# Performance work log

Measured on AMD Instinct MI355X. Metric: run time of the kernel, lower is better.

## Reference

```python
import jax, jax.numpy as jnp
import numpy as np

DIM = 768
NUM_HEADS = 12
HEAD_DIM = DIM // NUM_HEADS
SCALE = HEAD_DIM ** -0.5


def setup_inputs() -> dict:
    key = jax.random.key(0)
    k_x, k_qkv, k_proj, k_pb = jax.random.split(key, 4)
    B, N = 4, 2048
    x = jax.random.normal(k_x, (B, N, DIM), dtype=jnp.float32)
    # torch.nn.Linear stores weight as [out_features, in_features]
    w_qkv = jax.random.normal(k_qkv, (3 * DIM, DIM), dtype=jnp.float32) * (DIM ** -0.5)
    w_proj = jax.random.normal(k_proj, (DIM, DIM), dtype=jnp.float32) * (DIM ** -0.5)
    b_proj = jax.random.normal(k_pb, (DIM,), dtype=jnp.float32) * 0.02
    return {"x": x, "w_qkv": w_qkv, "w_proj": w_proj, "b_proj": b_proj}


def reference(x, w_qkv, w_proj, b_proj):
    B, N, C = x.shape
    # qkv projection (no bias): [B, N, 3*C]
    qkv = jnp.einsum('bnc,dc->bnd', x, w_qkv)
    qkv = qkv.reshape(B, N, 3, NUM_HEADS, HEAD_DIM)
    qkv = jnp.transpose(qkv, (2, 0, 3, 1, 4))  # [3, B, H, N, hd]
    q, k, v = qkv[0], qkv[1], qkv[2]
    q = q * SCALE
    attn = jnp.einsum('bhqd,bhkd->bhqk', q, k)          # [B, H, N, N]
    attn = jax.nn.softmax(attn, axis=-1)
    out = jnp.einsum('bhqk,bhkd->bhqd', attn, v)        # [B, H, N, hd]
    out = jnp.transpose(out, (0, 2, 1, 3)).reshape(B, N, C)
    return jnp.einsum('bnc,dc->bnd', out, w_proj) + b_proj
```

## Files before the change

kernel.cpp:

```cpp
#include <hip/hip_runtime.h>

typedef unsigned short u16;
typedef unsigned int u32;
typedef __attribute__((ext_vector_type(4))) unsigned short u16x4;
typedef __attribute__((ext_vector_type(8))) short short8;
typedef __attribute__((ext_vector_type(4))) float f32x4;
typedef __attribute__((ext_vector_type(8))) float f32x8;
typedef __attribute__((ext_vector_type(2))) unsigned int u32x2;

#define MFMA(a, b, c) __builtin_amdgcn_mfma_f32_16x16x32_bf16((a), (b), (c), 0, 0, 0)

__device__ __forceinline__ u16 f2bf(float f) {
    union { float f; unsigned int u; } v; v.f = f;
    unsigned int u = v.u;
    return (u16)((u + 0x7fffu + ((u >> 16) & 1u)) >> 16);
}

__device__ __forceinline__ float exp2fast(float x) {
#if __has_builtin(__builtin_amdgcn_exp2f)
    return __builtin_amdgcn_exp2f(x);
#else
    return exp2f(x);
#endif
}

__device__ __forceinline__ unsigned int cvtpk(float lo, float hi) {
    unsigned int r;
    asm("v_cvt_pk_bf16_f32 %0, %1, %2" : "=v"(r) : "v"(lo), "v"(hi));
    return r;
}

__device__ __forceinline__ void gload16(const void* g, void* l) {
    __builtin_amdgcn_global_load_lds((const __attribute__((address_space(1))) unsigned int*)g,
                                     (__attribute__((address_space(3))) unsigned int*)l,
                                     16, 0, 0);
}

#define N1 6291456
#define N2 1769472
#define N3 589824

__global__ __launch_bounds__(256) void cvt_bf16(const float* __restrict__ x,
                                                const float* __restrict__ wq,
                                                const float* __restrict__ wp,
                                                u16* __restrict__ xb,
                                                u16* __restrict__ wqb,
                                                u16* __restrict__ wpb) {
    size_t i = ((size_t)blockIdx.x * 256 + threadIdx.x) * 8;
    const float* src;
    u16* dst;
    size_t off;
    if (i < N1)            { src = x;  dst = xb;  off = i; }
    else if (i < N1 + N2)  { src = wq; dst = wqb; off = i - N1; }
    else                   { src = wp; dst = wpb; off = i - N1 - N2; }
    f32x8 v = *(const f32x8*)(src + off);
    short8 o;
#pragma unroll
    for (int j = 0; j < 8; ++j) o[j] = (short)f2bf(v[j]);
    *(short8*)(dst + off) = o;
}

__global__ __launch_bounds__(256) void qkv_gemm(const u16* __restrict__ X,
                                                const u16* __restrict__ W,
                                                u16* __restrict__ Qb,
                                                u16* __restrict__ Kb,
                                                u16* __restrict__ Vt) {
    __shared__ __align__(16) u16 abuf[128 * 64];
    __shared__ __align__(16) u16 bbuf[128 * 64];

    const int id = blockIdx.x;
    const int swz = (id & 7) * 144 + (id >> 3);
    const int m0 = (swz & 63) * 128;
    const int n0 = (swz >> 6) * 128;
    const int tid = threadIdx.x;
    const int lane = tid & 63;
    const int w = tid >> 6;
    const int wm = (w >> 1) * 64, wn = (w & 1) * 64;
    const int lrow = lane & 15, rgrp = lane >> 4;

    const int sr = lane >> 3;
    const int schunk = (lane & 7) ^ (sr & 7);
    const u16* asrc = X + (size_t)(m0 + w * 32 + sr) * 768 + schunk * 8;
    const u16* bsrc = W + (size_t)(n0 + w * 32 + sr) * 768 + schunk * 8;
    u16* adst = abuf + (w * 32) * 64;
    u16* bdst = bbuf + (w * 32) * 64;

    f32x4 acc[4][4] = {};

    for (int k0 = 0; k0 < 768; k0 += 64) {
        __syncthreads();
#pragma unroll
        for (int p = 0; p < 4; ++p) {
            gload16(asrc + (size_t)(p * 8) * 768 + k0, adst + (p * 8) * 64);
            gload16(bsrc + (size_t)(p * 8) * 768 + k0, bdst + (p * 8) * 64);
        }
        __syncthreads();

        __builtin_amdgcn_s_setprio(1);
#pragma unroll
        for (int ks = 0; ks < 2; ++ks) {
            short8 a[4], b[4];
            const int cs = (ks * 4 + rgrp);
#pragma unroll
            for (int mf = 0; mf < 4; ++mf)
                a[mf] = *(const short8*)(abuf + (wm + mf * 16 + lrow) * 64 + ((cs ^ (lrow & 7)) * 8));
#pragma unroll
            for (int nf = 0; nf < 4; ++nf)
                b[nf] = *(const short8*)(bbuf + (wn + nf * 16 + lrow) * 64 + ((cs ^ (lrow & 7)) * 8));
#pragma unroll
            for (int mf = 0; mf < 4; ++mf)
#pragma unroll
                for (int nf = 0; nf < 4; ++nf)
                    acc[mf][nf] = MFMA(a[mf], b[nf], acc[mf][nf]);
        }
        __builtin_amdgcn_s_setprio(0);
    }

    const int which = n0 / 768;
    if (which < 2) {
        u16* dst = (which == 0) ? Qb : Kb;
        const float scl = (which == 0) ? 0.180336879f : 1.0f;
#pragma unroll
        for (int mf = 0; mf < 4; ++mf)
#pragma unroll
            for (int nf = 0; nf < 4; ++nf)
#pragma unroll
                for (int r = 0; r < 4; ++r) {
                    int m = m0 + wm + mf * 16 + rgrp * 4 + r;
                    int d = n0 + wn + nf * 16 + lrow - which * 768;
                    int h = d >> 6, e = d & 63;
                    int bb = m >> 11, nseq = m & 2047;
                    dst[(((size_t)bb * 12 + h) * 2048 + nseq) * 64 + e] = f2bf(acc[mf][nf][r] * scl);
                }
    } else {
#pragma unroll
        for (int mf = 0; mf < 4; ++mf) {
            const int m = m0 + wm + mf * 16 + rgrp * 4;
            const int bb = m >> 11, nseq = m & 2047;
#pragma unroll
            for (int nf = 0; nf < 4; ++nf) {
                const int d = n0 + wn + nf * 16 + lrow - 1536;
                const int h = d >> 6, e = d & 63;
                u16x4 v4;
#pragma unroll
                for (int r = 0; r < 4; ++r) v4[r] = f2bf(acc[mf][nf][r]);
                *(u16x4*)(Vt + ((((size_t)bb * 12 + h) * 64 + e) * 2048 + nseq)) = v4;
            }
        }
    }
}

__global__ __launch_bounds__(512) void attn_kernel(const u16* __restrict__ Qb,
                                                   const u16* __restrict__ Kb,
                                                   const u16* __restrict__ Vt,
                                                   u16* __restrict__ AO) {
    __shared__ __align__(16) u16 kbuf[2][4096];
    __shared__ __align__(16) u16 vbuf[2][4096];
    __shared__ __align__(16) u16 pbuf[8][16 * 72];

    const int id = blockIdx.x;
    const int xcd = id & 7, per = id >> 3;
    const int bh = xcd * 6 + (per >> 4);
    const int q0 = (per & 15) * 128;
    const int tid = threadIdx.x;
    const int lane = tid & 63;
    const int w = tid >> 6;
    const int lrow = lane & 15, rgrp = lane >> 4, lk = rgrp * 8;

    const u16* Qp = Qb + (size_t)bh * 2048 * 64;
    const u16* Kp = Kb + (size_t)bh * 2048 * 64;
    const u16* Vp = Vt + (size_t)bh * 64 * 2048;

    const int srow = w * 8 + (lane >> 3);
    const int schunk = lane & 7;
    const int sswz = schunk ^ (srow & 7);
    const u16* ksrc = Kp + srow * 64 + sswz * 8;
    const u16* vsrc = Vp + (size_t)srow * 2048 + sswz * 8;
    const int woff = w * 512;

    const int row0 = q0 + w * 16;
    short8 qf[2];
#pragma unroll
    for (int ks = 0; ks < 2; ++ks)
        qf[ks] = *(const short8*)(Qp + (size_t)(row0 + lrow) * 64 + ks * 32 + lk);

    f32x4 oacc[4] = {};
    float lrun = 0.f;

    u16* Pw = pbuf[w];
    const int swz = lane & 7;

    gload16(ksrc, kbuf[0] + woff);
    gload16(vsrc, vbuf[0] + woff);

    for (int kt = 0; kt < 32; ++kt) {
        const int cur = kt & 1;
        __syncthreads();
        if (kt + 1 < 32) {
            gload16(ksrc + (kt + 1) * 4096, kbuf[cur ^ 1] + woff);
            gload16(vsrc + (kt + 1) * 64,   vbuf[cur ^ 1] + woff);
        }

        const u16* kb = kbuf[cur];
        f32x4 sacc[4];
#pragma unroll
        for (int nf = 0; nf < 4; ++nf) sacc[nf] = f32x4{-16.f, -16.f, -16.f, -16.f};
        __builtin_amdgcn_s_setprio(1);
#pragma unroll
        for (int nf = 0; nf < 4; ++nf)
#pragma unroll
            for (int ks = 0; ks < 2; ++ks) {
                short8 kf = *(const short8*)(kb + (nf * 16 + lrow) * 64 + ((ks * 4 + rgrp) ^ swz) * 8);
                sacc[nf] = MFMA(kf, qf[ks], sacc[nf]);
            }
        __builtin_amdgcn_s_setprio(0);

#pragma unroll
        for (int nf = 0; nf < 4; ++nf) {
            float p0 = exp2fast(sacc[nf][0]);
            float p1 = exp2fast(sacc[nf][1]);
            float p2 = exp2fast(sacc[nf][2]);
            float p3 = exp2fast(sacc[nf][3]);
            lrun += (p0 + p1) + (p2 + p3);
            u32x2 pk;
            pk.x = cvtpk(p0, p1);
            pk.y = cvtpk(p2, p3);
            *(u32x2*)&Pw[lrow * 72 + nf * 16 + rgrp * 4] = pk;
        }

        const u16* vb = vbuf[cur];
        __builtin_amdgcn_s_setprio(1);
#pragma unroll
        for (int ks = 0; ks < 2; ++ks) {
            short8 pa = *(const short8*)&Pw[lrow * 72 + ks * 32 + lk];
#pragma unroll
            for (int df = 0; df < 4; ++df) {
                short8 vf = *(const short8*)(vb + (df * 16 + lrow) * 64 + ((ks * 4 + rgrp) ^ swz) * 8);
                oacc[df] = MFMA(pa, vf, oacc[df]);
            }
        }
        __builtin_amdgcn_s_setprio(0);
    }

    float l = lrun;
    l += __shfl_xor(l, 16);
    l += __shfl_xor(l, 32);
    float linv[4];
#pragma unroll
    for (int r = 0; r < 4; ++r) linv[r] = 1.f / __shfl(l, rgrp * 4 + r);

    const int b = bh / 12, h = bh % 12;
#pragma unroll
    for (int r = 0; r < 4; ++r) {
        int row = row0 + rgrp * 4 + r;
#pragma unroll
        for (int df = 0; df < 4; ++df)
            AO[((size_t)b * 2048 + row) * 768 + h * 64 + df * 16 + lrow] = f2bf(oacc[df][r] * linv[r]);
    }
}

__global__ __launch_bounds__(256) void proj_gemm(const u16* __restrict__ A,
                                                 const u16* __restrict__ W,
                                                 const float* __restrict__ bias,
                                                 float* __restrict__ out) {
    __shared__ __align__(16) u16 abuf[64 * 64];
    __shared__ __align__(16) u16 bbuf[128 * 64];

    const int id = blockIdx.x;
    const int swz = (id & 7) * 96 + (id >> 3);
    const int m0 = (swz & 127) * 64;
    const int n0 = (swz >> 7) * 128;
    const int tid = threadIdx.x;
    const int lane = tid & 63;
    const int w = tid >> 6;
    const int lrow = lane & 15, rgrp = lane >> 4;

    const int sra = w * 16 + (lane >> 3);
    const int srb = w * 32 + (lane >> 3);
    const int aswz = (lane & 7) ^ (sra & 7);
    const int bswz = (lane & 7) ^ (srb & 7);
    const u16* asrc = A + (size_t)(m0 + sra) * 768 + aswz * 8;
    const u16* bsrc = W + (size_t)(n0 + srb) * 768 + bswz * 8;
    u16* adst0 = abuf + (w * 16) * 64;
    u16* bdst0 = bbuf + (w * 32) * 64;

    f32x4 acc[4][2] = {};

    for (int k0 = 0; k0 < 768; k0 += 64) {
        __syncthreads();
#pragma unroll
        for (int p = 0; p < 2; ++p)
            gload16(asrc + (size_t)(p * 8) * 768 + k0, adst0 + (p * 8) * 64);
#pragma unroll
        for (int p = 0; p < 4; ++p)
            gload16(bsrc + (size_t)(p * 8) * 768 + k0, bdst0 + (p * 8) * 64);
        __syncthreads();

        __builtin_amdgcn_s_setprio(1);
#pragma unroll
        for (int ks = 0; ks < 2; ++ks) {
            short8 a[4], b[2];
            const int cs = (ks * 4 + rgrp);
#pragma unroll
            for (int mf = 0; mf < 4; ++mf)
                a[mf] = *(const short8*)(abuf + (mf * 16 + lrow) * 64 + ((cs ^ (lrow & 7)) * 8));
#pragma unroll
            for (int nf = 0; nf < 2; ++nf)
                b[nf] = *(const short8*)(bbuf + (w * 32 + nf * 16 + lrow) * 64 + ((cs ^ (lrow & 7)) * 8));
#pragma unroll
            for (int mf = 0; mf < 4; ++mf)
#pragma unroll
                for (int nf = 0; nf < 2; ++nf)
                    acc[mf][nf] = MFMA(a[mf], b[nf], acc[mf][nf]);
        }
        __builtin_amdgcn_s_setprio(0);
    }

#pragma unroll
    for (int nf = 0; nf < 2; ++nf) {
        const int d = n0 + w * 32 + nf * 16 + lrow;
        const float bv = bias[d];
#pragma unroll
        for (int mf = 0; mf < 4; ++mf)
#pragma unroll
            for (int r = 0; r < 4; ++r) {
                const int m = m0 + mf * 16 + rgrp * 4 + r;
                out[(size_t)m * 768 + d] = acc[mf][nf][r] + bv;
            }
    }
}

extern "C" void kernel_launch(void* const* d_in, const int* in_sizes, int n_in,
                              void* d_out, int out_size, void* d_ws, size_t ws_size,
                              hipStream_t stream) {
    const float* x      = (const float*)d_in[0];
    const float* w_qkv  = (const float*)d_in[1];
    const float* w_proj = (const float*)d_in[2];
    const float* b_proj = (const float*)d_in[3];
    float* out = (float*)d_out;

    const size_t per = (size_t)48 * 2048 * 64;
    u16* Qb  = (u16*)d_ws;
    u16* Kb  = Qb + per;
    u16* Vt  = Kb + per;
    u16* XB  = Vt + per;
    u16* AO  = XB;
    u16* WQB = XB + per;
    u16* WPB = WQB + (size_t)N2;

    cvt_bf16<<<4224, 256, 0, stream>>>(x, w_qkv, w_proj, XB, WQB, WPB);
    qkv_gemm<<<1152, 256, 0, stream>>>(XB, WQB, Qb, Kb, Vt);
    attn_kernel<<<768, 512, 0, stream>>>(Qb, Kb, Vt, AO);
    proj_gemm<<<768, 256, 0, stream>>>(AO, WPB, b_proj, out);
}
```

Before: 146.5 us.

## Double-buffer LDS tiles with K-step 32 in QKV and projection GEMMs

Both GEMMs now use two LDS buffers with a K-step of 32 instead of a single buffer with K-step 64. The next tile's global-to-LDS load is issued right after one barrier, before the current tile's MFMAs run, so one of the two barriers per iteration goes away and loads overlap compute. A new XOR swizzle fits the 32-wide rows. The trade-off is twice as many loop iterations with fewer MFMAs each, and correctness depends on the gload16 completion semantics before the next barrier.

```diff
diff --git a/kernel.cpp b/kernel.cpp
--- a/kernel.cpp
+++ b/kernel.cpp
@@ -65,8 +65,8 @@
                                                 u16* __restrict__ Qb,
                                                 u16* __restrict__ Kb,
                                                 u16* __restrict__ Vt) {
-    __shared__ __align__(16) u16 abuf[128 * 64];
-    __shared__ __align__(16) u16 bbuf[128 * 64];
+    __shared__ __align__(16) u16 abuf[2 * 4096];
+    __shared__ __align__(16) u16 bbuf[2 * 4096];
 
     const int id = blockIdx.x;
     const int swz = (id & 7) * 144 + (id >> 3);
@@ -78,43 +78,49 @@
     const int wm = (w >> 1) * 64, wn = (w & 1) * 64;
     const int lrow = lane & 15, rgrp = lane >> 4;
 
-    const int sr = lane >> 3;
-    const int schunk = (lane & 7) ^ (sr & 7);
-    const u16* asrc = X + (size_t)(m0 + w * 32 + sr) * 768 + schunk * 8;
-    const u16* bsrc = W + (size_t)(n0 + w * 32 + sr) * 768 + schunk * 8;
-    u16* adst = abuf + (w * 32) * 64;
-    u16* bdst = bbuf + (w * 32) * 64;
+    const int fs = ((lane >> 2) & 3) ^ ((lane >> 4) & 3);
+    const int sc = (lane & 3) ^ fs;
+    const u16* asrc = X + (size_t)(m0 + w * 32 + (lane >> 2)) * 768 + sc * 8;
+    const u16* bsrc = W + (size_t)(n0 + w * 32 + (lane >> 2)) * 768 + sc * 8;
+
+    const int fr = (lrow & 3) ^ ((lrow >> 2) & 3);
+    const int ca = (rgrp ^ fr) * 8;
 
     f32x4 acc[4][4] = {};
 
-    for (int k0 = 0; k0 < 768; k0 += 64) {
+#define QSTAGE(B, T)                                                          \
+    do {                                                                      \
+        const int kk = (T) * 32;                                              \
+        gload16(asrc + kk,            abuf + (B) * 4096 + (w * 32) * 32);     \
+        gload16(asrc + 16 * 768 + kk, abuf + (B) * 4096 + (w * 32 + 16) * 32);\
+        gload16(bsrc + kk,            bbuf + (B) * 4096 + (w * 32) * 32);     \
+        gload16(bsrc + 16 * 768 + kk, bbuf + (B) * 4096 + (w * 32 + 16) * 32);\
+    } while (0)
+
+    QSTAGE(0, 0);
+    for (int t = 0; t < 24; ++t) {
+        const int cur = t & 1;
         __syncthreads();
-#pragma unroll
-        for (int p = 0; p < 4; ++p) {
-            gload16(asrc + (size_t)(p * 8) * 768 + k0, adst + (p * 8) * 64);
-            gload16(bsrc + (size_t)(p * 8) * 768 + k0, bdst + (p * 8) * 64);
-        }
-        __syncthreads();
-
+        if (t < 23) QSTAGE(cur ^ 1, t + 1);
+
+        const u16* ab = abuf + cur * 4096;
+        const u16* bb = bbuf + cur * 4096;
+        short8 a[4], b[4];
+#pragma unroll
+        for (int mf = 0; mf < 4; ++mf)
+            a[mf] = *(const short8*)(ab + (wm + mf * 16 + lrow) * 32 + ca);
+#pragma unroll
+        for (int nf = 0; nf < 4; ++nf)
+            b[nf] = *(const short8*)(bb + (wn + nf * 16 + lrow) * 32 + ca);
         __builtin_amdgcn_s_setprio(1);
 #pragma unroll
-        for (int ks = 0; ks < 2; ++ks) {
-            short8 a[4], b[4];
-            const int cs = (ks * 4 + rgrp);
-#pragma unroll
-            for (int mf = 0; mf < 4; ++mf)
-                a[mf] = *(const short8*)(abuf + (wm + mf * 16 + lrow) * 64 + ((cs ^ (lrow & 7)) * 8));
+        for (int mf = 0; mf < 4; ++mf)
 #pragma unroll
             for (int nf = 0; nf < 4; ++nf)
-                b[nf] = *(const short8*)(bbuf + (wn + nf * 16 + lrow) * 64 + ((cs ^ (lrow & 7)) * 8));
-#pragma unroll
-            for (int mf = 0; mf < 4; ++mf)
-#pragma unroll
-                for (int nf = 0; nf < 4; ++nf)
-                    acc[mf][nf] = MFMA(a[mf], b[nf], acc[mf][nf]);
-        }
+                acc[mf][nf] = MFMA(a[mf], b[nf], acc[mf][nf]);
         __builtin_amdgcn_s_setprio(0);
     }
+#undef QSTAGE
 
     const int which = n0 / 768;
     if (which < 2) {
@@ -129,14 +135,14 @@
                     int m = m0 + wm + mf * 16 + rgrp * 4 + r;
                     int d = n0 + wn + nf * 16 + lrow - which * 768;
                     int h = d >> 6, e = d & 63;
-                    int bb = m >> 11, nseq = m & 2047;
-                    dst[(((size_t)bb * 12 + h) * 2048 + nseq) * 64 + e] = f2bf(acc[mf][nf][r] * scl);
+                    int bb2 = m >> 11, nseq = m & 2047;
+                    dst[(((size_t)bb2 * 12 + h) * 2048 + nseq) * 64 + e] = f2bf(acc[mf][nf][r] * scl);
                 }
     } else {
 #pragma unroll
         for (int mf = 0; mf < 4; ++mf) {
             const int m = m0 + wm + mf * 16 + rgrp * 4;
-            const int bb = m >> 11, nseq = m & 2047;
+            const int bb2 = m >> 11, nseq = m & 2047;
 #pragma unroll
             for (int nf = 0; nf < 4; ++nf) {
                 const int d = n0 + wn + nf * 16 + lrow - 1536;
@@ -144,7 +150,7 @@
                 u16x4 v4;
 #pragma unroll
                 for (int r = 0; r < 4; ++r) v4[r] = f2bf(acc[mf][nf][r]);
-                *(u16x4*)(Vt + ((((size_t)bb * 12 + h) * 64 + e) * 2048 + nseq)) = v4;
+                *(u16x4*)(Vt + ((((size_t)bb2 * 12 + h) * 64 + e) * 2048 + nseq)) = v4;
             }
         }
     }
@@ -263,8 +269,8 @@
                                                  const u16* __restrict__ W,
                                                  const float* __restrict__ bias,
                                                  float* __restrict__ out) {
-    __shared__ __align__(16) u16 abuf[64 * 64];
-    __shared__ __align__(16) u16 bbuf[128 * 64];
+    __shared__ __align__(16) u16 abuf[2 * 2048];
+    __shared__ __align__(16) u16 bbuf[2 * 4096];
 
     const int id = blockIdx.x;
     const int swz = (id & 7) * 96 + (id >> 3);
@@ -275,46 +281,48 @@
     const int w = tid >> 6;
     const int lrow = lane & 15, rgrp = lane >> 4;
 
-    const int sra = w * 16 + (lane >> 3);
-    const int srb = w * 32 + (lane >> 3);
-    const int aswz = (lane & 7) ^ (sra & 7);
-    const int bswz = (lane & 7) ^ (srb & 7);
-    const u16* asrc = A + (size_t)(m0 + sra) * 768 + aswz * 8;
-    const u16* bsrc = W + (size_t)(n0 + srb) * 768 + bswz * 8;
-    u16* adst0 = abuf + (w * 16) * 64;
-    u16* bdst0 = bbuf + (w * 32) * 64;
+    const int fs = ((lane >> 2) & 3) ^ ((lane >> 4) & 3);
+    const int sc = (lane & 3) ^ fs;
+    const u16* asrc = A + (size_t)(m0 + w * 16 + (lane >> 2)) * 768 + sc * 8;
+    const u16* bsrc = W + (size_t)(n0 + w * 32 + (lane >> 2)) * 768 + sc * 8;
+
+    const int fr = (lrow & 3) ^ ((lrow >> 2) & 3);
+    const int ca = (rgrp ^ fr) * 8;
 
     f32x4 acc[4][2] = {};
 
-    for (int k0 = 0; k0 < 768; k0 += 64) {
+#define PSTAGE(B, T)                                                          \
+    do {                                                                      \
+        const int kk = (T) * 32;                                              \
+        gload16(asrc + kk,            abuf + (B) * 2048 + (w * 16) * 32);     \
+        gload16(bsrc + kk,            bbuf + (B) * 4096 + (w * 32) * 32);     \
+        gload16(bsrc + 16 * 768 + kk, bbuf + (B) * 4096 + (w * 32 + 16) * 32);\
+    } while (0)
+
+    PSTAGE(0, 0);
+    for (int t = 0; t < 24; ++t) {
+        const int cur = t & 1;
         __syncthreads();
-#pragma unroll
-        for (int p = 0; p < 2; ++p)
-            gload16(asrc + (size_t)(p * 8) * 768 + k0, adst0 + (p * 8) * 64);
-#pragma unroll
-        for (int p = 0; p < 4; ++p)
-            gload16(bsrc + (size_t)(p * 8) * 768 + k0, bdst0 + (p * 8) * 64);
-        __syncthreads();
-
+        if (t < 23) PSTAGE(cur ^ 1, t + 1);
+
+        const u16* ab = abuf + cur * 2048;
+        const u16* bb = bbuf + cur * 4096;
+        short8 a[4], b[2];
+#pragma unroll
+        for (int mf = 0; mf < 4; ++mf)
+            a[mf] = *(const short8*)(ab + (mf * 16 + lrow) * 32 + ca);
+#pragma unroll
+        for (int nf = 0; nf < 2; ++nf)
+            b[nf] = *(const short8*)(bb + (w * 32 + nf * 16 + lrow) * 32 + ca);
         __builtin_amdgcn_s_setprio(1);
 #pragma unroll
-        for (int ks = 0; ks < 2; ++ks) {
-            short8 a[4], b[2];
-            const int cs = (ks * 4 + rgrp);
-#pragma unroll
-            for (int mf = 0; mf < 4; ++mf)
-                a[mf] = *(const short8*)(abuf + (mf * 16 + lrow) * 64 + ((cs ^ (lrow & 7)) * 8));
+        for (int mf = 0; mf < 4; ++mf)
 #pragma unroll
             for (int nf = 0; nf < 2; ++nf)
-                b[nf] = *(const short8*)(bbuf + (w * 32 + nf * 16 + lrow) * 64 + ((cs ^ (lrow & 7)) * 8));
-#pragma unroll
-            for (int mf = 0; mf < 4; ++mf)
-#pragma unroll
-                for (int nf = 0; nf < 2; ++nf)
-                    acc[mf][nf] = MFMA(a[mf], b[nf], acc[mf][nf]);
-        }
+                acc[mf][nf] = MFMA(a[mf], b[nf], acc[mf][nf]);
         __builtin_amdgcn_s_setprio(0);
     }
+#undef PSTAGE
 
 #pragma unroll
     for (int nf = 0; nf < 2; ++nf) {
```

After: 159.7 us. 9.0% more time.

## Double-buffer LDS tiles in QKV and output projection GEMMs

Applied to the files above, without the earlier changes.

Both GEMM kernels now keep two LDS stages for the A and B tiles. The next K-tile's global-to-LDS loads are issued right after the barrier, before the MFMA work on the current tile, and each iteration needs one barrier instead of two. The aim is to hide global load latency behind matrix math. In exchange, LDS per block doubles (64 KB for qkv_gemm), which may reduce how many blocks fit on each CU.

```diff
diff --git a/kernel.cpp b/kernel.cpp
--- a/kernel.cpp
+++ b/kernel.cpp
@@ -65,8 +65,8 @@
                                                 u16* __restrict__ Qb,
                                                 u16* __restrict__ Kb,
                                                 u16* __restrict__ Vt) {
-    __shared__ __align__(16) u16 abuf[128 * 64];
-    __shared__ __align__(16) u16 bbuf[128 * 64];
+    __shared__ __align__(16) u16 abuf[2 * 8192];
+    __shared__ __align__(16) u16 bbuf[2 * 8192];
 
     const int id = blockIdx.x;
     const int swz = (id & 7) * 144 + (id >> 3);
@@ -82,20 +82,29 @@
     const int schunk = (lane & 7) ^ (sr & 7);
     const u16* asrc = X + (size_t)(m0 + w * 32 + sr) * 768 + schunk * 8;
     const u16* bsrc = W + (size_t)(n0 + w * 32 + sr) * 768 + schunk * 8;
-    u16* adst = abuf + (w * 32) * 64;
-    u16* bdst = bbuf + (w * 32) * 64;
 
     f32x4 acc[4][4] = {};
 
-    for (int k0 = 0; k0 < 768; k0 += 64) {
+#define QSTAGE(B, T)                                                            \
+    do {                                                                        \
+        const int kk = (T) * 64;                                                \
+        _Pragma("unroll")                                                       \
+        for (int p = 0; p < 4; ++p) {                                           \
+            gload16(asrc + (size_t)(p * 8) * 768 + kk,                          \
+                    abuf + (B) * 8192 + (w * 32 + p * 8) * 64);                 \
+            gload16(bsrc + (size_t)(p * 8) * 768 + kk,                          \
+                    bbuf + (B) * 8192 + (w * 32 + p * 8) * 64);                 \
+        }                                                                       \
+    } while (0)
+
+    QSTAGE(0, 0);
+    for (int t = 0; t < 12; ++t) {
+        const int cur = t & 1;
         __syncthreads();
-#pragma unroll
-        for (int p = 0; p < 4; ++p) {
-            gload16(asrc + (size_t)(p * 8) * 768 + k0, adst + (p * 8) * 64);
-            gload16(bsrc + (size_t)(p * 8) * 768 + k0, bdst + (p * 8) * 64);
-        }
-        __syncthreads();
-
+        if (t < 11) QSTAGE(cur ^ 1, t + 1);
+
+        const u16* ab = abuf + cur * 8192;
+        const u16* bb = bbuf + cur * 8192;
         __builtin_amdgcn_s_setprio(1);
 #pragma unroll
         for (int ks = 0; ks < 2; ++ks) {
@@ -103,10 +112,10 @@
             const int cs = (ks * 4 + rgrp);
 #pragma unroll
             for (int mf = 0; mf < 4; ++mf)
-                a[mf] = *(const short8*)(abuf + (wm + mf * 16 + lrow) * 64 + ((cs ^ (lrow & 7)) * 8));
+                a[mf] = *(const short8*)(ab + (wm + mf * 16 + lrow) * 64 + ((cs ^ (lrow & 7)) * 8));
 #pragma unroll
             for (int nf = 0; nf < 4; ++nf)
-                b[nf] = *(const short8*)(bbuf + (wn + nf * 16 + lrow) * 64 + ((cs ^ (lrow & 7)) * 8));
+                b[nf] = *(const short8*)(bb + (wn + nf * 16 + lrow) * 64 + ((cs ^ (lrow & 7)) * 8));
 #pragma unroll
             for (int mf = 0; mf < 4; ++mf)
 #pragma unroll
@@ -115,6 +124,7 @@
         }
         __builtin_amdgcn_s_setprio(0);
     }
+#undef QSTAGE
 
     const int which = n0 / 768;
     if (which < 2) {
@@ -129,14 +139,14 @@
                     int m = m0 + wm + mf * 16 + rgrp * 4 + r;
                     int d = n0 + wn + nf * 16 + lrow - which * 768;
                     int h = d >> 6, e = d & 63;
-                    int bb = m >> 11, nseq = m & 2047;
-                    dst[(((size_t)bb * 12 + h) * 2048 + nseq) * 64 + e] = f2bf(acc[mf][nf][r] * scl);
+                    int bb2 = m >> 11, nseq = m & 2047;
+                    dst[(((size_t)bb2 * 12 + h) * 2048 + nseq) * 64 + e] = f2bf(acc[mf][nf][r] * scl);
                 }
     } else {
 #pragma unroll
         for (int mf = 0; mf < 4; ++mf) {
             const int m = m0 + wm + mf * 16 + rgrp * 4;
-            const int bb = m >> 11, nseq = m & 2047;
+            const int bb2 = m >> 11, nseq = m & 2047;
 #pragma unroll
             for (int nf = 0; nf < 4; ++nf) {
                 const int d = n0 + wn + nf * 16 + lrow - 1536;
@@ -144,7 +154,7 @@
                 u16x4 v4;
 #pragma unroll
                 for (int r = 0; r < 4; ++r) v4[r] = f2bf(acc[mf][nf][r]);
-                *(u16x4*)(Vt + ((((size_t)bb * 12 + h) * 64 + e) * 2048 + nseq)) = v4;
+                *(u16x4*)(Vt + ((((size_t)bb2 * 12 + h) * 64 + e) * 2048 + nseq)) = v4;
             }
         }
     }
@@ -263,8 +273,8 @@
                                                  const u16* __restrict__ W,
                                                  const float* __restrict__ bias,
                                                  float* __restrict__ out) {
-    __shared__ __align__(16) u16 abuf[64 * 64];
-    __shared__ __align__(16) u16 bbuf[128 * 64];
+    __shared__ __align__(16) u16 abuf[2 * 4096];
+    __shared__ __align__(16) u16 bbuf[2 * 8192];
 
     const int id = blockIdx.x;
     const int swz = (id & 7) * 96 + (id >> 3);
@@ -281,21 +291,30 @@
     const int bswz = (lane & 7) ^ (srb & 7);
     const u16* asrc = A + (size_t)(m0 + sra) * 768 + aswz * 8;
     const u16* bsrc = W + (size_t)(n0 + srb) * 768 + bswz * 8;
-    u16* adst0 = abuf + (w * 16) * 64;
-    u16* bdst0 = bbuf + (w * 32) * 64;
 
     f32x4 acc[4][2] = {};
 
-    for (int k0 = 0; k0 < 768; k0 += 64) {
+#define PSTAGE(B, T)                                                            \
+    do {                                                                        \
+        const int kk = (T) * 64;                                                \
+        _Pragma("unroll")                                                       \
+        for (int p = 0; p < 2; ++p)                                             \
+            gload16(asrc + (size_t)(p * 8) * 768 + kk,                          \
+                    abuf + (B) * 4096 + (w * 16 + p * 8) * 64);                 \
+        _Pragma("unroll")                                                       \
+        for (int p = 0; p < 4; ++p)                                             \
+            gload16(bsrc + (size_t)(p * 8) * 768 + kk,                          \
+                    bbuf + (B) * 8192 + (w * 32 + p * 8) * 64);                 \
+    } while (0)
+
+    PSTAGE(0, 0);
+    for (int t = 0; t < 12; ++t) {
+        const int cur = t & 1;
         __syncthreads();
-#pragma unroll
-        for (int p = 0; p < 2; ++p)
-            gload16(asrc + (size_t)(p * 8) * 768 + k0, adst0 + (p * 8) * 64);
-#pragma unroll
-        for (int p = 0; p < 4; ++p)
-            gload16(bsrc + (size_t)(p * 8) * 768 + k0, bdst0 + (p * 8) * 64);
-        __syncthreads();
-
+        if (t < 11) PSTAGE(cur ^ 1, t + 1);
+
+        const u16* ab = abuf + cur * 4096;
+        const u16* bb = bbuf + cur * 8192;
         __builtin_amdgcn_s_setprio(1);
 #pragma unroll
         for (int ks = 0; ks < 2; ++ks) {
@@ -303,10 +322,10 @@
             const int cs = (ks * 4 + rgrp);
 #pragma unroll
             for (int mf = 0; mf < 4; ++mf)
-                a[mf] = *(const short8*)(abuf + (mf * 16 + lrow) * 64 + ((cs ^ (lrow & 7)) * 8));
+                a[mf] = *(const short8*)(ab + (mf * 16 + lrow) * 64 + ((cs ^ (lrow & 7)) * 8));
 #pragma unroll
             for (int nf = 0; nf < 2; ++nf)
-                b[nf] = *(const short8*)(bbuf + (w * 32 + nf * 16 + lrow) * 64 + ((cs ^ (lrow & 7)) * 8));
+                b[nf] = *(const short8*)(bb + (w * 32 + nf * 16 + lrow) * 64 + ((cs ^ (lrow & 7)) * 8));
 #pragma unroll
             for (int mf = 0; mf < 4; ++mf)
 #pragma unroll
@@ -315,6 +334,7 @@
         }
         __builtin_amdgcn_s_setprio(0);
     }
+#undef PSTAGE
 
 #pragma unroll
     for (int nf = 0; nf < 2; ++nf) {
```

Result: slower. 150.6 us (+2.8%).
